# Performance work log

Measured on AMD Instinct MI355X. Metric: run time of the kernel, lower is better.

## Reference

```python
import jax, jax.numpy as jnp
import numpy as np

B, T, C = 256, 256, 384
HEADS = 6
HEAD_DIM = C // HEADS
WINDOW = 64


def setup_inputs() -> dict:
    key = jax.random.key(0)
    ks = jax.random.split(key, 5)
    scale = 0.02
    return {
        "x": jax.random.normal(ks[0], (B, T, C), dtype=jnp.float32),
        "qkv_w": jax.random.normal(ks[1], (C, 3 * C), dtype=jnp.float32) * scale,
        "qkv_b": jax.random.normal(ks[2], (3 * C,), dtype=jnp.float32) * scale,
        "proj_w": jax.random.normal(ks[3], (C, C), dtype=jnp.float32) * scale,
        "proj_b": jax.random.normal(ks[4], (C,), dtype=jnp.float32) * scale,
        "gate": jnp.ones((C,), dtype=jnp.float32),
    }


def reference(x, qkv_w, qkv_b, proj_w, proj_b, gate):
    Bx, Tx, Cx = x.shape
    qkv = x @ qkv_w + qkv_b                     # [B, T, 3C]
    q, k, v = jnp.split(qkv, 3, axis=-1)
    # [B, T, H, hd] -> [B, H, T, hd]
    q = q.reshape(Bx, Tx, HEADS, HEAD_DIM).transpose(0, 2, 1, 3)
    k = k.reshape(Bx, Tx, HEADS, HEAD_DIM).transpose(0, 2, 1, 3)
    v = v.reshape(Bx, Tx, HEADS, HEAD_DIM).transpose(0, 2, 1, 3)

    att = jnp.einsum("bhqd,bhkd->bhqk", q, k) * (1.0 / np.sqrt(HEAD_DIM).astype(np.float32))
    idx = jnp.arange(Tx)
    causal = idx[:, None] >= idx[None, :]                 # j <= i
    local = jnp.abs(idx[:, None] - idx[None, :]) <= WINDOW
    mask = (causal & local)[None, None, :, :]             # [1,1,T,T]
    att = jnp.where(mask, att, -jnp.inf)
    att = jax.nn.softmax(att, axis=-1)

    out = jnp.einsum("bhqk,bhkd->bhqd", att, v)           # [B, H, T, hd]
    out = out.transpose(0, 2, 1, 3).reshape(Bx, Tx, Cx)
    return (out * gate) @ proj_w + proj_b
```

## Files before the change

kernel.cpp:

```cpp
#include <hip/hip_runtime.h>
#include <hip/hip_bf16.h>

typedef unsigned short u16;
typedef __attribute__((ext_vector_type(8))) short short8;
typedef __attribute__((ext_vector_type(8))) unsigned short ushort8;
typedef __attribute__((ext_vector_type(4))) float f32x4;
typedef __attribute__((ext_vector_type(4))) float f4;

#define GLB_CAST(p) ((const __attribute__((address_space(1))) unsigned int*)(p))
#define LDS_CAST(p) ((__attribute__((address_space(3))) unsigned int*)(p))

__device__ __forceinline__ void gl_lds16(const void* g, void* l) {
  __builtin_amdgcn_global_load_lds(GLB_CAST(g), LDS_CAST(l), 16, 0, 0);
}

__device__ __forceinline__ u16 f2bf(float f) {
  __hip_bfloat16 b = __float2bfloat16(f);
  return __builtin_bit_cast(u16, b);
}

__global__ void transpose_cvt_k(const float* __restrict__ in,
                                u16* __restrict__ out, int R, int C) {
  __shared__ float tile[32][33];
  int c0 = blockIdx.x * 32, r0 = blockIdx.y * 32;
  int tx = threadIdx.x, ty = threadIdx.y;
#pragma unroll
  for (int i = 0; i < 32; i += 8)
    tile[ty + i][tx] = in[(size_t)(r0 + ty + i) * C + c0 + tx];
  __syncthreads();
#pragma unroll
  for (int i = 0; i < 32; i += 8)
    out[(size_t)(c0 + ty + i) * R + r0 + tx] = f2bf(tile[tx][ty + i]);
}

template <int EPI>
__global__ __launch_bounds__(512, 1) void gemm_k(
    const void* __restrict__ Av, const u16* __restrict__ Bt,
    const float* __restrict__ bias,
    u16* __restrict__ oQ, u16* __restrict__ oK, u16* __restrict__ oV,
    float* __restrict__ oF) {
  constexpr int K = 384;
  constexpr int NT = (EPI == 1) ? 9 : 3;
  __shared__ u16 As[128 * 384];
  __shared__ u16 Bring[3][128 * 64];
  __shared__ float bias_s[NT * 128];

  const int tid = threadIdx.x;
  const int m0 = blockIdx.x * 128;

  for (int i = tid; i < NT * 128; i += 512) bias_s[i] = bias[i];

  const int br = tid >> 3;
  const int bcs = ((tid & 7) ^ (br & 7)) * 8;
  auto stageB = [&](int slot, int tn, int kt) {
    const u16* s = Bt + (size_t)(tn * 128 + br) * K + kt * 64 + bcs;
    gl_lds16(s, (char*)Bring[slot] + tid * 16);
    gl_lds16(s + (size_t)64 * K, (char*)Bring[slot] + tid * 16 + 8192);
  };

  stageB(0, 0, 0);
  stageB(1, 0, 1);

  if (EPI == 1) {
    const float* X = (const float*)Av;
#pragma unroll
    for (int i = 0; i < 12; ++i) {
      int c = tid + i * 512;
      int row = c / 48, cc = c % 48;
      const float* src = X + (size_t)(m0 + row) * K + cc * 8;
      f4 a = *(const f4*)src;
      f4 b = *(const f4*)(src + 4);
      ushort8 o;
#pragma unroll
      for (int j = 0; j < 4; ++j) { o[j] = f2bf(a[j]); o[4 + j] = f2bf(b[j]); }
      *(ushort8*)((char*)As + row * 768 + ((cc * 16) ^ ((row & 7) << 4))) = o;
    }
  } else {
    const u16* Ab = (const u16*)Av;
#pragma unroll
    for (int i = 0; i < 12; ++i) {
      int c = tid + i * 512;
      int row = c / 48, cc = c % 48;
      int cs = cc ^ (row & 7);
      gl_lds16(Ab + (size_t)(m0 + row) * K + cs * 8, (char*)As + c * 16);
    }
  }
  __syncthreads();

  const int lane = tid & 63, wid = tid >> 6;
  const int lo = lane & 15, hi = lane >> 4;
  const int wr = wid >> 2, wc = wid & 3;
  const int akey = (lo & 7) << 4;
  int abase[4];
#pragma unroll
  for (int m = 0; m < 4; ++m) abase[m] = (wr * 64 + m * 16 + lo) * 768;
  const int bbase = (wc * 32 + lo) * 128;

  const f32x4 Z4 = {0.f, 0.f, 0.f, 0.f};

  for (int t = 0; t < NT; ++t) {
    float bs[2];
    bs[0] = bias_s[t * 128 + wc * 32 + lo];
    bs[1] = bias_s[t * 128 + wc * 32 + 16 + lo];
    f32x4 acc[4][2];
#pragma unroll
    for (int m = 0; m < 4; ++m) { acc[m][0] = Z4; acc[m][1] = Z4; }

#pragma unroll
    for (int kt = 0; kt < 6; ++kt) {
      if (kt == 5) asm volatile("s_waitcnt vmcnt(0)" ::: "memory");
      else         asm volatile("s_waitcnt vmcnt(2)" ::: "memory");
      __builtin_amdgcn_s_barrier();
      __builtin_amdgcn_sched_barrier(0);

      const char* bB = (const char*)Bring[kt % 3];
      short8 af[4][2], bf[2][2];
#pragma unroll
      for (int m = 0; m < 4; ++m)
#pragma unroll
        for (int s = 0; s < 2; ++s)
          af[m][s] = *(const short8*)((const char*)As + abase[m] +
                                      ((kt * 128 + s * 64 + hi * 16) ^ akey));
#pragma unroll
      for (int n = 0; n < 2; ++n)
#pragma unroll
        for (int s = 0; s < 2; ++s)
          bf[n][s] = *(const short8*)(bB + bbase + n * 2048 +
                                      ((s * 64 + hi * 16) ^ akey));

      if (kt < 4) stageB((kt + 2) % 3, t, kt + 2);

      __builtin_amdgcn_s_setprio(1);
#pragma unroll
      for (int s = 0; s < 2; ++s)
#pragma unroll
        for (int m = 0; m < 4; ++m)
#pragma unroll
          for (int n = 0; n < 2; ++n)
            acc[m][n] = __builtin_amdgcn_mfma_f32_16x16x32_bf16(
                af[m][s], bf[n][s], acc[m][n], 0, 0, 0);
      __builtin_amdgcn_s_setprio(0);
    }

    if (EPI == 1) {
      const int region = t / 3;
      u16* dst = (region == 0) ? oQ : ((region == 1) ? oK : oV);
      const int colb = (t % 3) * 128 + wc * 32 + lo;
#pragma unroll
      for (int n = 0; n < 2; ++n) {
        int hc = colb + n * 16;
        int hh = hc >> 6, d = hc & 63;
#pragma unroll
        for (int m = 0; m < 4; ++m)
#pragma unroll
          for (int rr = 0; rr < 4; ++rr) {
            int gm = m0 + wr * 64 + m * 16 + hi * 4 + rr;
            dst[(((size_t)((gm >> 8) * 6 + hh) << 8 | (gm & 255)) << 6) + d] =
                f2bf(acc[m][n][rr] + bs[n]);
          }
      }
    } else {
      const int colb = t * 128 + wc * 32 + lo;
#pragma unroll
      for (int m = 0; m < 4; ++m)
#pragma unroll
        for (int rr = 0; rr < 4; ++rr) {
          int gm = m0 + wr * 64 + m * 16 + hi * 4 + rr;
#pragma unroll
          for (int n = 0; n < 2; ++n)
            oF[(size_t)gm * 384 + colb + n * 16] = acc[m][n][rr] + bs[n];
        }
    }

    if (t + 1 < NT) {
      stageB(0, t + 1, 0);
      stageB(1, t + 1, 1);
    }
  }
}

__global__ __launch_bounds__(256) void attn_k(
    const u16* __restrict__ Qb, const u16* __restrict__ Kb,
    const u16* __restrict__ Vb, const float* __restrict__ gate,
    u16* __restrict__ Ao) {
  __shared__ u16 Ks[128 * 64];
  __shared__ u16 Vs[64 * 128];
  __shared__ u16 Ps[4][16 * 128];
  const int bx = blockIdx.x;
  const int qt = bx & 3, bh = bx >> 2;
  const int h = bh % 6, b = bh / 6;
  const int i0 = qt * 64, j0 = i0 - 64;
  const int tid = threadIdx.x, w = tid >> 6, lane = tid & 63;
  const int lo = lane & 15, hi = lane >> 4;

  const u16* Kh = Kb + (size_t)bh * (256 * 64);
  const u16* Vh = Vb + (size_t)bh * (256 * 64);
  const u16* Qh = Qb + (size_t)bh * (256 * 64);

#pragma unroll
  for (int it = 0; it < 4; ++it) {
    int chunk = tid + it * 256;
    int row = chunk >> 3, cc = chunk & 7;
    int csrc = cc ^ (row & 7);
    int j = j0 + row; if (j < 0) j = 0;
    gl_lds16(Kh + j * 64 + csrc * 8, Ks + chunk * 8);
  }
#pragma unroll
  for (int it = 0; it < 4; ++it) {
    int c = tid + it * 256;
    int dc = c >> 7;
    int j = c & 127;
    int jj = j0 + j; if (jj < 0) jj = 0;
    ushort8 v = *(const ushort8*)(Vh + jj * 64 + dc * 8);
#pragma unroll
    for (int e = 0; e < 8; ++e) {
      int d = dc * 8 + e;
      *(u16*)((char*)Vs + ((d * 256 + 2 * j) ^ ((d & 7) << 4))) = v[e];
    }
  }

  const int iq = i0 + w * 16 + lo;
  short8 aq0 = *(const short8*)(Qh + iq * 64 + hi * 8);
  short8 aq1 = *(const short8*)(Qh + iq * 64 + 32 + hi * 8);

  __syncthreads();

  const f32x4 Z4 = {0.f, 0.f, 0.f, 0.f};
  f32x4 accS[8];
#pragma unroll
  for (int t = 0; t < 8; ++t) accS[t] = Z4;
#pragma unroll
  for (int t = 0; t < 8; ++t) {
    int key = t * 16 + lo;
    int base = key * 128;
    int sw = (key & 7) << 4;
    short8 bk0 = *(const short8*)((const char*)Ks + ((base + hi * 16) ^ sw));
    short8 bk1 = *(const short8*)((const char*)Ks + ((base + 64 + hi * 16) ^ sw));
    accS[t] = __builtin_amdgcn_mfma_f32_16x16x32_bf16(aq0, bk0, accS[t], 0, 0, 0);
    accS[t] = __builtin_amdgcn_mfma_f32_16x16x32_bf16(aq1, bk1, accS[t], 0, 0, 0);
  }

  float pv[4][8];
  float rinv[4];
#pragma unroll
  for (int r = 0; r < 4; ++r) {
    int i = i0 + w * 16 + hi * 4 + r;
    float mx = -1e30f;
    float vals[8];
#pragma unroll
    for (int t = 0; t < 8; ++t) {
      int j = j0 + t * 16 + lo;
      float s = accS[t][r] * 0.125f;
      bool ok = (j >= 0) && (j <= i) && (j >= i - 64);
      vals[t] = ok ? s : -1e30f;
      mx = fmaxf(mx, vals[t]);
    }
#pragma unroll
    for (int off = 1; off < 16; off <<= 1) mx = fmaxf(mx, __shfl_xor(mx, off));
    float sum = 0.f;
#pragma unroll
    for (int t = 0; t < 8; ++t) {
      float p = __expf(vals[t] - mx);
      pv[r][t] = p;
      sum += p;
    }
#pragma unroll
    for (int off = 1; off < 16; off <<= 1) sum += __shfl_xor(sum, off);
    rinv[r] = 1.0f / sum;
  }

  u16* Pw = Ps[w];
#pragma unroll
  for (int r = 0; r < 4; ++r) {
    int ql = hi * 4 + r;
    int sw = (ql & 7) << 4;
#pragma unroll
    for (int t = 0; t < 8; ++t) {
      int off = (ql * 256 + (t * 16 + lo) * 2) ^ sw;
      *(u16*)((char*)Pw + off) = f2bf(pv[r][t]);
    }
  }

  f32x4 accO[4];
#pragma unroll
  for (int dt = 0; dt < 4; ++dt) accO[dt] = Z4;
#pragma unroll
  for (int ks = 0; ks < 4; ++ks) {
    int offA = (lo * 256 + ks * 64 + hi * 16) ^ ((lo & 7) << 4);
    short8 ap = *(const short8*)((const char*)Pw + offA);
#pragma unroll
    for (int dt = 0; dt < 4; ++dt) {
      int d = dt * 16 + lo;
      int offB = (d * 256 + ks * 64 + hi * 16) ^ ((d & 7) << 4);
      short8 bv = *(const short8*)((const char*)Vs + offB);
      accO[dt] = __builtin_amdgcn_mfma_f32_16x16x32_bf16(ap, bv, accO[dt], 0, 0, 0);
    }
  }

#pragma unroll
  for (int dt = 0; dt < 4; ++dt) {
    int d = dt * 16 + lo;
    float gg = gate[h * 64 + d];
#pragma unroll
    for (int r = 0; r < 4; ++r) {
      int i = i0 + w * 16 + hi * 4 + r;
      float v = accO[dt][r] * rinv[r] * gg;
      Ao[(size_t)(b * 256 + i) * 384 + h * 64 + d] = f2bf(v);
    }
  }
}

extern "C" void kernel_launch(void* const* d_in, const int* in_sizes, int n_in,
                              void* d_out, int out_size, void* d_ws, size_t ws_size,
                              hipStream_t stream) {
  const float* x      = (const float*)d_in[0];
  const float* qkv_w  = (const float*)d_in[1];
  const float* qkv_b  = (const float*)d_in[2];
  const float* proj_w = (const float*)d_in[3];
  const float* proj_b = (const float*)d_in[4];
  const float* gate   = (const float*)d_in[5];
  float* out = (float*)d_out;

  char* ws = (char*)d_ws;
  u16* att  = (u16*)ws;
  u16* vbuf = (u16*)(ws + 50331648);
  u16* w1T  = (u16*)(ws + 100663296);
  u16* pT   = (u16*)(ws + 101548032);
  u16* qbuf = (u16*)d_out;
  u16* kbuf = (u16*)((char*)d_out + 50331648);

  transpose_cvt_k<<<dim3(1152 / 32, 384 / 32), dim3(32, 8), 0, stream>>>(qkv_w, w1T, 384, 1152);
  transpose_cvt_k<<<dim3(384 / 32, 384 / 32), dim3(32, 8), 0, stream>>>(proj_w, pT, 384, 384);

  gemm_k<1><<<512, 512, 0, stream>>>(x, w1T, qkv_b, qbuf, kbuf, vbuf, nullptr);
  attn_k<<<256 * 6 * 4, 256, 0, stream>>>(qbuf, kbuf, vbuf, gate, att);
  gemm_k<2><<<512, 512, 0, stream>>>(att, pT, proj_b, nullptr, nullptr, nullptr, out);
}
```

Before: 199.8 us.

## Give each GEMM wave a private B staging ring and drop per-step block barriers

Each wave now loads only the 32 B columns it consumes into its own triple-buffered LDS slice, with K steps of 32. This removes the block-wide s_barrier on every K step, because waves synchronize only through their own vmcnt waits. Prefetch of the next N tile's first B chunks now wraps across tile boundaries instead of stalling after the epilogue. Epilogue row offsets are also precomputed once. The catch is twice as many K iterations with smaller MFMA batches per wait, and the B tile is loaded redundantly across the wr wave rows.

Result: no change. 196.5 us (-1.7%).

```diff
diff --git a/kernel.cpp b/kernel.cpp
--- a/kernel.cpp
+++ b/kernel.cpp
@@ -42,20 +42,25 @@
   constexpr int K = 384;
   constexpr int NT = (EPI == 1) ? 9 : 3;
   __shared__ u16 As[128 * 384];
-  __shared__ u16 Bring[3][128 * 64];
+  __shared__ u16 Bs[8][3][1024];
   __shared__ float bias_s[NT * 128];
 
   const int tid = threadIdx.x;
   const int m0 = blockIdx.x * 128;
+  const int lane = tid & 63, wid = tid >> 6;
+  const int lo = lane & 15, hi = lane >> 4;
+  const int wr = wid >> 2, wc = wid & 3;
 
   for (int i = tid; i < NT * 128; i += 512) bias_s[i] = bias[i];
 
-  const int br = tid >> 3;
-  const int bcs = ((tid & 7) ^ (br & 7)) * 8;
+  const int bcol = wc * 32 + (lane >> 2);
+  const int bko = (lane & 3) * 8;
+  char* const slot_l = (char*)&Bs[0][0][0] + wid * 6144 + lane * 16;
   auto stageB = [&](int slot, int tn, int kt) {
-    const u16* s = Bt + (size_t)(tn * 128 + br) * K + kt * 64 + bcs;
-    gl_lds16(s, (char*)Bring[slot] + tid * 16);
-    gl_lds16(s + (size_t)64 * K, (char*)Bring[slot] + tid * 16 + 8192);
+    const u16* s = Bt + (size_t)(tn * 128 + bcol) * K + kt * 32 + bko;
+    char* d = slot_l + slot * 2048;
+    gl_lds16(s, d);
+    gl_lds16(s + 16 * K, d + 1024);
   };
 
   stageB(0, 0, 0);
@@ -87,94 +92,81 @@
   }
   __syncthreads();
 
-  const int lane = tid & 63, wid = tid >> 6;
-  const int lo = lane & 15, hi = lane >> 4;
-  const int wr = wid >> 2, wc = wid & 3;
   const int akey = (lo & 7) << 4;
   int abase[4];
 #pragma unroll
   for (int m = 0; m < 4; ++m) abase[m] = (wr * 64 + m * 16 + lo) * 768;
-  const int bbase = (wc * 32 + lo) * 128;
+  const int bbase = lo * 64 + hi * 16;
+  const char* const Asc = (const char*)As;
+  const char* const sb0 = (const char*)&Bs[0][0][0] + wid * 6144;
+
+  int rp[4][4];
+#pragma unroll
+  for (int m = 0; m < 4; ++m)
+#pragma unroll
+    for (int rr = 0; rr < 4; ++rr) {
+      int gm = m0 + wr * 64 + m * 16 + hi * 4 + rr;
+      rp[m][rr] = (EPI == 1) ? ((gm >> 8) * 98304 + (gm & 255) * 64)
+                             : gm * 384;
+    }
 
   const f32x4 Z4 = {0.f, 0.f, 0.f, 0.f};
 
   for (int t = 0; t < NT; ++t) {
-    float bs[2];
-    bs[0] = bias_s[t * 128 + wc * 32 + lo];
-    bs[1] = bias_s[t * 128 + wc * 32 + 16 + lo];
     f32x4 acc[4][2];
 #pragma unroll
     for (int m = 0; m < 4; ++m) { acc[m][0] = Z4; acc[m][1] = Z4; }
 
 #pragma unroll
-    for (int kt = 0; kt < 6; ++kt) {
-      if (kt == 5) asm volatile("s_waitcnt vmcnt(0)" ::: "memory");
+    for (int kt = 0; kt < 12; ++kt) {
+      if (kt == 0) asm volatile("s_waitcnt vmcnt(4)" ::: "memory");
       else         asm volatile("s_waitcnt vmcnt(2)" ::: "memory");
-      __builtin_amdgcn_s_barrier();
-      __builtin_amdgcn_sched_barrier(0);
-
-      const char* bB = (const char*)Bring[kt % 3];
-      short8 af[4][2], bf[2][2];
+
+      const char* sb = sb0 + (kt % 3) * 2048;
+      short8 af[4], bf[2];
 #pragma unroll
       for (int m = 0; m < 4; ++m)
-#pragma unroll
-        for (int s = 0; s < 2; ++s)
-          af[m][s] = *(const short8*)((const char*)As + abase[m] +
-                                      ((kt * 128 + s * 64 + hi * 16) ^ akey));
-#pragma unroll
-      for (int n = 0; n < 2; ++n)
-#pragma unroll
-        for (int s = 0; s < 2; ++s)
-          bf[n][s] = *(const short8*)(bB + bbase + n * 2048 +
-                                      ((s * 64 + hi * 16) ^ akey));
-
-      if (kt < 4) stageB((kt + 2) % 3, t, kt + 2);
+        af[m] = *(const short8*)(Asc + abase[m] + ((kt * 64 + hi * 16) ^ akey));
+      bf[0] = *(const short8*)(sb + bbase);
+      bf[1] = *(const short8*)(sb + 1024 + bbase);
+
+      if (kt < 10)           stageB((kt + 2) % 3, t, kt + 2);
+      else if (t + 1 < NT)   stageB((kt + 2) % 3, t + 1, kt - 10);
 
       __builtin_amdgcn_s_setprio(1);
 #pragma unroll
-      for (int s = 0; s < 2; ++s)
-#pragma unroll
-        for (int m = 0; m < 4; ++m)
-#pragma unroll
-          for (int n = 0; n < 2; ++n)
-            acc[m][n] = __builtin_amdgcn_mfma_f32_16x16x32_bf16(
-                af[m][s], bf[n][s], acc[m][n], 0, 0, 0);
+      for (int m = 0; m < 4; ++m) {
+        acc[m][0] = __builtin_amdgcn_mfma_f32_16x16x32_bf16(af[m], bf[0], acc[m][0], 0, 0, 0);
+        acc[m][1] = __builtin_amdgcn_mfma_f32_16x16x32_bf16(af[m], bf[1], acc[m][1], 0, 0, 0);
+      }
       __builtin_amdgcn_s_setprio(0);
     }
 
+    float bs0 = bias_s[t * 128 + wc * 32 + lo];
+    float bs1 = bias_s[t * 128 + wc * 32 + 16 + lo];
     if (EPI == 1) {
-      const int region = t / 3;
-      u16* dst = (region == 0) ? oQ : ((region == 1) ? oK : oV);
-      const int colb = (t % 3) * 128 + wc * 32 + lo;
-#pragma unroll
-      for (int n = 0; n < 2; ++n) {
-        int hc = colb + n * 16;
-        int hh = hc >> 6, d = hc & 63;
-#pragma unroll
-        for (int m = 0; m < 4; ++m)
-#pragma unroll
-          for (int rr = 0; rr < 4; ++rr) {
-            int gm = m0 + wr * 64 + m * 16 + hi * 4 + rr;
-            dst[(((size_t)((gm >> 8) * 6 + hh) << 8 | (gm & 255)) << 6) + d] =
-                f2bf(acc[m][n][rr] + bs[n]);
-          }
-      }
+      int r3 = t / 3;
+      u16* dst = (r3 == 0) ? oQ : ((r3 == 1) ? oK : oV);
+      int hc0 = (t - r3 * 3) * 128 + wc * 32 + lo;
+      int cp0 = ((hc0 >> 6) << 14) + (hc0 & 63);
+      int hc1 = hc0 + 16;
+      int cp1 = ((hc1 >> 6) << 14) + (hc1 & 63);
+#pragma unroll
+      for (int m = 0; m < 4; ++m)
+#pragma unroll
+        for (int rr = 0; rr < 4; ++rr) {
+          dst[(size_t)(rp[m][rr] + cp0)] = f2bf(acc[m][0][rr] + bs0);
+          dst[(size_t)(rp[m][rr] + cp1)] = f2bf(acc[m][1][rr] + bs1);
+        }
     } else {
-      const int colb = t * 128 + wc * 32 + lo;
+      int colb = t * 128 + wc * 32 + lo;
 #pragma unroll
       for (int m = 0; m < 4; ++m)
 #pragma unroll
         for (int rr = 0; rr < 4; ++rr) {
-          int gm = m0 + wr * 64 + m * 16 + hi * 4 + rr;
-#pragma unroll
-          for (int n = 0; n < 2; ++n)
-            oF[(size_t)gm * 384 + colb + n * 16] = acc[m][n][rr] + bs[n];
+          oF[(size_t)(rp[m][rr] + colb)] = acc[m][0][rr] + bs0;
+          oF[(size_t)(rp[m][rr] + colb + 16)] = acc[m][1][rr] + bs1;
         }
-    }
-
-    if (t + 1 < NT) {
-      stageB(0, t + 1, 0);
-      stageB(1, t + 1, 1);
     }
   }
 }
```
